# Kernel tuning notes

Measured on AMD Instinct MI355X. Metric: run time of the kernel, lower is better.

The kernel has to match this reference:

```python
import jax, jax.numpy as jnp
import numpy as np

EPS = 1e-8
LAMB = 0.5
L2_NORM = 1e-4
NUM_USERS = 100000
NUM_ITEMS = 50000
EMBED = 64
R = 3
NNZ = 1_000_000
IG_NNZ = 500_000
B = 512
K = 100


def _spmm(rows, cols, vals, X, num_rows):
    # sparse [num_rows, n] @ X  via gather + segment-sum
    return jax.ops.segment_sum(X[cols] * vals[:, None], rows, num_segments=num_rows)


def setup_inputs() -> dict:
    key = jax.random.key(0)
    ks = jax.random.split(key, 16)
    user = jax.random.randint(ks[0], (B,), 0, NUM_USERS)
    item = jax.random.randint(ks[1], (B, K), 0, NUM_ITEMS)
    rel_rows = jax.random.randint(ks[2], (R, NNZ), 0, NUM_USERS)
    rel_cols = jax.random.randint(ks[3], (R, NNZ), 0, NUM_ITEMS)
    ig_rows = jax.random.randint(ks[4], (R, IG_NNZ), 0, NUM_ITEMS)
    ig_cols = jax.random.randint(ks[5], (R, IG_NNZ), 0, NUM_ITEMS)
    ig_vals = jnp.ones((R, IG_NNZ), jnp.float32)
    train_rows = jax.random.randint(ks[6], (NNZ,), 0, NUM_USERS)
    train_cols = jax.random.randint(ks[7], (NNZ,), 0, NUM_ITEMS)
    user_embedding = 0.1 * jax.random.normal(ks[8], (NUM_USERS, EMBED), jnp.float32)
    item_embedding = 0.1 * jax.random.normal(ks[9], (NUM_ITEMS, EMBED), jnp.float32)
    mgnn_weight = jnp.ones((R,), jnp.float32)
    item_behavior_W = 0.05 * jax.random.normal(ks[10], (R, 2 * EMBED, 2 * EMBED), jnp.float32)
    item_propagate_W = 0.05 * jax.random.normal(ks[11], (R, EMBED, EMBED), jnp.float32)
    W = 0.05 * jax.random.normal(ks[12], (EMBED, EMBED), jnp.float32)
    return {"user": user, "item": item, "rel_rows": rel_rows, "rel_cols": rel_cols,
            "ig_rows": ig_rows, "ig_cols": ig_cols, "ig_vals": ig_vals,
            "train_rows": train_rows, "train_cols": train_cols,
            "user_embedding": user_embedding, "item_embedding": item_embedding,
            "mgnn_weight": mgnn_weight, "item_behavior_W": item_behavior_W,
            "item_propagate_W": item_propagate_W, "W": W}


def reference(user, item, rel_rows, rel_cols, ig_rows, ig_cols, ig_vals,
              train_rows, train_cols, user_embedding, item_embedding,
              mgnn_weight, item_behavior_W, item_propagate_W, W):
    # user behavior degree [U, R] (number of interactions per user per relation)
    ub_deg = jax.vmap(lambda r: jax.ops.segment_sum(
        jnp.ones(r.shape, jnp.float32), r, num_segments=NUM_USERS))(rel_rows).T
    total_weight = ub_deg @ mgnn_weight[:, None]                       # [U,1]
    user_behavior_weight = ub_deg * mgnn_weight[None, :] / (total_weight + EPS)

    user_feature = jnp.zeros((NUM_USERS, EMBED), user_embedding.dtype)
    score2 = jnp.zeros((item.shape[0], item.shape[1]), user_embedding.dtype)
    for i in range(R):
        # item-item propagation for relation i
        ig_deg = jax.ops.segment_sum(ig_vals[i], ig_rows[i], num_segments=NUM_ITEMS)[:, None]
        item_agg = _spmm(ig_rows[i], ig_cols[i], ig_vals[i], item_embedding, NUM_ITEMS)
        item_agg = item_agg / (ig_deg + EPS)
        tmp_item_prop = jnp.concatenate([item_embedding, item_agg @ item_propagate_W[i]], axis=1)  # [I,2E]

        ones = jnp.ones(rel_rows[i].shape, user_embedding.dtype)
        ub_d = ub_deg[:, i:i + 1]
        tmp_user_neigh = _spmm(rel_rows[i], rel_cols[i], ones, item_embedding, NUM_USERS) / (ub_d + EPS)
        tmp_user_item_p = _spmm(rel_rows[i], rel_cols[i], ones, tmp_item_prop, NUM_USERS) / (ub_d + EPS)

        user_feature = user_feature + user_behavior_weight[:, i:i + 1] * tmp_user_neigh
        proj = tmp_user_item_p @ item_behavior_W[i]                    # [U,2E]
        # score2 term: <proj[user], tmp_item_prop[item]> per candidate
        score2 = score2 + jnp.einsum('be,bke->bk', proj[user], tmp_item_prop[item])
    score2 = score2 / R

    # item feature from transposed train matrix (values=1, no node dropout)
    item_feature = jax.ops.segment_sum(user_embedding[train_rows], train_cols, num_segments=NUM_ITEMS)

    uf = jnp.concatenate([user_embedding, user_feature @ W], axis=1)   # [U,2E]
    itf = jnp.concatenate([item_embedding, item_feature @ W], axis=1)  # [I,2E]

    u_g = uf[user]                                                     # [B,2E]
    i_g = itf[item]                                                    # [B,K,2E]
    score1 = jnp.einsum('be,bke->bk', u_g, i_g)
    scores = score1 + LAMB * score2
    # L2 on expanded user feature [B,K,2E] and gathered item feature
    l2_loss = L2_NORM * (item.shape[1] * (u_g ** 2).sum() + (i_g ** 2).sum())
    return scores, l2_loss
```

## Files before the change

### kernel.cpp

```cpp
#include <hip/hip_runtime.h>

#define EPSF     1e-8f
#define LAMBF    0.5f
#define L2NORMF  1e-4f
#define NUSERS   100000
#define NITEMS   50000
#define EMB      64
#define RREL     3
#define NNZ_     1000000
#define IGNNZ    500000
#define BB       512
#define KK       100

#define IGTOT    (RREL * IGNNZ)
#define TOTE     (IGTOT + NNZ_)
#define NBIN_SEG 782
#define NBINS    (4 * NBIN_SEG)
#define NBLK     128
#define BTH      1024
#define SLICE    ((TOTE + NBLK - 1) / NBLK)
#define CAPE     2048
#define GTH      512

__global__ void scatter_maps(const int* __restrict__ user, const int* __restrict__ item,
                             int* __restrict__ slot, int* __restrict__ iflag) {
    int i = blockIdx.x * blockDim.x + threadIdx.x;
    if (i < BB) slot[user[i]] = i;
    if (i < BB * KK) iflag[item[i]] = 1;
}

__device__ __forceinline__ int edge_bin(int i, const int* ig_rows, const int* train_cols) {
    if (i < IGTOT) return (i / IGNNZ) * NBIN_SEG + (ig_rows[i] >> 6);
    return 3 * NBIN_SEG + (train_cols[i - IGTOT] >> 6);
}

__global__ void pass1_count(const int* __restrict__ ig_rows, const int* __restrict__ train_cols,
                            int* __restrict__ pcnt) {
    __shared__ int h[NBINS];
    int b = blockIdx.x, t = threadIdx.x;
    for (int i = t; i < NBINS; i += BTH) h[i] = 0;
    __syncthreads();
    int s = b * SLICE, e = min(s + SLICE, TOTE);
    for (int i = s + t; i < e; i += BTH)
        atomicAdd(&h[edge_bin(i, ig_rows, train_cols)], 1);
    __syncthreads();
    for (int i = t; i < NBINS; i += BTH) pcnt[b * NBINS + i] = h[i];
}

__global__ void scan_tot(const int* __restrict__ pcnt, int* __restrict__ tot) {
    int bin = blockIdx.x * blockDim.x + threadIdx.x;
    if (bin >= NBINS) return;
    int s = 0;
    for (int b = 0; b < NBLK; b++) s += pcnt[b * NBINS + bin];
    tot[bin] = s;
}

__global__ void scan_bins(const int* __restrict__ tot, int* __restrict__ binbase) {
    __shared__ int csum[1024];
    int t = threadIdx.x;
    int base = t * 4;
    int v0 = (base + 0 < NBINS) ? tot[base + 0] : 0;
    int v1 = (base + 1 < NBINS) ? tot[base + 1] : 0;
    int v2 = (base + 2 < NBINS) ? tot[base + 2] : 0;
    int v3 = (base + 3 < NBINS) ? tot[base + 3] : 0;
    int s = v0 + v1 + v2 + v3;
    csum[t] = s;
    __syncthreads();
    for (int d = 1; d < 1024; d <<= 1) {
        int x = (t >= d) ? csum[t - d] : 0;
        __syncthreads();
        csum[t] += x;
        __syncthreads();
    }
    int run = csum[t] - s;
    if (base + 0 < NBINS) { binbase[base + 0] = run; run += v0; }
    if (base + 1 < NBINS) { binbase[base + 1] = run; run += v1; }
    if (base + 2 < NBINS) { binbase[base + 2] = run; run += v2; }
    if (base + 3 < NBINS) { binbase[base + 3] = run; run += v3; }
    if (t == 0) binbase[NBINS] = TOTE;
}

__global__ void scan_obase(const int* __restrict__ pcnt, const int* __restrict__ binbase,
                           int* __restrict__ obase) {
    int bin = blockIdx.x * blockDim.x + threadIdx.x;
    if (bin >= NBINS) return;
    int run = binbase[bin];
    for (int b = 0; b < NBLK; b++) {
        obase[b * NBINS + bin] = run;
        run += pcnt[b * NBINS + bin];
    }
}

__global__ void pass2_scatter(const int* __restrict__ ig_rows, const int* __restrict__ ig_cols,
                              const float* __restrict__ ig_vals, const int* __restrict__ train_rows,
                              const int* __restrict__ train_cols, const int* __restrict__ obase,
                              int2* __restrict__ garr, int* __restrict__ tcol) {
    __shared__ int pos[NBINS];
    int b = blockIdx.x, t = threadIdx.x;
    for (int i = t; i < NBINS; i += BTH) pos[i] = obase[b * NBINS + i];
    __syncthreads();
    int s = b * SLICE, e = min(s + SLICE, TOTE);
    for (int i = s + t; i < e; i += BTH) {
        if (i < IGTOT) {
            int dest = ig_rows[i];
            int bin = (i / IGNNZ) * NBIN_SEG + (dest >> 6);
            int slot = atomicAdd(&pos[bin], 1);
            garr[slot] = make_int2((ig_cols[i] << 6) | (dest & 63),
                                   __float_as_int(ig_vals[i]));
        } else {
            int e2 = i - IGTOT;
            int dest = train_cols[e2];
            int bin = 3 * NBIN_SEG + (dest >> 6);
            int slot = atomicAdd(&pos[bin], 1);
            tcol[slot - IGTOT] = (train_rows[e2] << 6) | (dest & 63);
        }
    }
}

__device__ __forceinline__ void bin_scan(int t, int* cnt, int* off, int* pos) {
    if (t < 64) {
        int v = cnt[t];
        int inc = v;
#pragma unroll
        for (int d = 1; d < 64; d <<= 1) {
            int x = __shfl_up(inc, d);
            if (t >= d) inc += x;
        }
        off[t] = inc - v;
        pos[t] = inc - v;
        if (t == 63) off[64] = inc;
    }
}

__global__ void ig_bin_gather(const float* __restrict__ item_emb, const int* __restrict__ binbase,
                              const int2* __restrict__ garr, float* __restrict__ prop2, int seg) {
    __shared__ int scol[CAPE];
    __shared__ float sval[CAPE];
    __shared__ int cnt[64], off[65], pos[64];
    int t = threadIdx.x, w = t >> 6, lane = t & 63;
    int bin = seg * NBIN_SEG + blockIdx.x;
    int bstart = binbase[bin], bend = binbase[bin + 1];
    int n = bend - bstart;
    int row0 = blockIdx.x * 64;
    if (n <= CAPE) {
        if (t < 64) cnt[t] = 0;
        __syncthreads();
        for (int i = t; i < n; i += GTH) atomicAdd(&cnt[garr[bstart + i].x & 63], 1);
        __syncthreads();
        bin_scan(t, cnt, off, pos);
        __syncthreads();
        for (int i = t; i < n; i += GTH) {
            int2 pv = garr[bstart + i];
            int sl = atomicAdd(&pos[pv.x & 63], 1);
            scol[sl] = pv.x >> 6;
            sval[sl] = __int_as_float(pv.y);
        }
        __syncthreads();
        for (int r = w; r < 64; r += 8) {
            int grow = row0 + r;
            if (grow >= NITEMS) break;
            int s = off[r], e = off[r + 1];
            float acc = 0.f, deg = 0.f;
            for (int k = s; k < e; k += 8) {
                int i0 = min(k + 0, e - 1), i1 = min(k + 1, e - 1);
                int i2 = min(k + 2, e - 1), i3 = min(k + 3, e - 1);
                int i4 = min(k + 4, e - 1), i5 = min(k + 5, e - 1);
                int i6 = min(k + 6, e - 1), i7 = min(k + 7, e - 1);
                int c0 = scol[i0], c1 = scol[i1], c2 = scol[i2], c3 = scol[i3];
                int c4 = scol[i4], c5 = scol[i5], c6 = scol[i6], c7 = scol[i7];
                float v0 = (k + 0 < e) ? sval[i0] : 0.f, v1 = (k + 1 < e) ? sval[i1] : 0.f;
                float v2 = (k + 2 < e) ? sval[i2] : 0.f, v3 = (k + 3 < e) ? sval[i3] : 0.f;
                float v4 = (k + 4 < e) ? sval[i4] : 0.f, v5 = (k + 5 < e) ? sval[i5] : 0.f;
                float v6 = (k + 6 < e) ? sval[i6] : 0.f, v7 = (k + 7 < e) ? sval[i7] : 0.f;
                float f0 = item_emb[c0 * 64 + lane], f1 = item_emb[c1 * 64 + lane];
                float f2 = item_emb[c2 * 64 + lane], f3 = item_emb[c3 * 64 + lane];
                float f4 = item_emb[c4 * 64 + lane], f5 = item_emb[c5 * 64 + lane];
                float f6 = item_emb[c6 * 64 + lane], f7 = item_emb[c7 * 64 + lane];
                acc += v0 * f0 + v1 * f1 + v2 * f2 + v3 * f3
                     + v4 * f4 + v5 * f5 + v6 * f6 + v7 * f7;
                deg += (v0 + v1 + v2 + v3) + (v4 + v5 + v6 + v7);
            }
            prop2[grow * 64 + lane] = acc / (deg + EPSF);
        }
    } else {
        for (int r = w; r < 64; r += 8) {
            int grow = row0 + r;
            if (grow >= NITEMS) break;
            float acc = 0.f, deg = 0.f;
            for (int j0 = bstart; j0 < bend; j0 += 64) {
                int j = j0 + lane;
                int2 pv = (j < bend) ? garr[j] : make_int2(-1, 0);
                unsigned long long mask = __ballot(pv.x >= 0 && (pv.x & 63) == r);
                while (mask) {
                    int jj = __builtin_ctzll(mask); mask &= mask - 1;
                    int pj = __shfl(pv.x, jj);
                    float vj = __shfl(__int_as_float(pv.y), jj);
                    acc += vj * item_emb[(pj >> 6) * 64 + lane];
                    deg += vj;
                }
            }
            prop2[grow * 64 + lane] = acc / (deg + EPSF);
        }
    }
}

__global__ void train_bin_gather(const float* __restrict__ user_emb, const int* __restrict__ binbase,
                                 const int* __restrict__ tcol, const int* __restrict__ iflag,
                                 float* __restrict__ itf2) {
    __shared__ int scol[CAPE];
    __shared__ int cnt[64], off[65], pos[64];
    int t = threadIdx.x, w = t >> 6, lane = t & 63;
    int bin = 3 * NBIN_SEG + blockIdx.x;
    int bstart = binbase[bin] - IGTOT, bend = binbase[bin + 1] - IGTOT;
    int n = bend - bstart;
    int row0 = blockIdx.x * 64;
    if (n <= CAPE) {
        if (t < 64) cnt[t] = 0;
        __syncthreads();
        for (int i = t; i < n; i += GTH) atomicAdd(&cnt[tcol[bstart + i] & 63], 1);
        __syncthreads();
        bin_scan(t, cnt, off, pos);
        __syncthreads();
        for (int i = t; i < n; i += GTH) {
            int p = tcol[bstart + i];
            int sl = atomicAdd(&pos[p & 63], 1);
            scol[sl] = p >> 6;
        }
        __syncthreads();
        for (int r = w; r < 64; r += 8) {
            int grow = row0 + r;
            if (grow >= NITEMS) break;
            if (!iflag[grow]) continue;
            int s = off[r], e = off[r + 1];
            float acc = 0.f;
            for (int k = s; k < e; k += 8) {
                int i0 = min(k + 0, e - 1), i1 = min(k + 1, e - 1);
                int i2 = min(k + 2, e - 1), i3 = min(k + 3, e - 1);
                int i4 = min(k + 4, e - 1), i5 = min(k + 5, e - 1);
                int i6 = min(k + 6, e - 1), i7 = min(k + 7, e - 1);
                int c0 = scol[i0], c1 = scol[i1], c2 = scol[i2], c3 = scol[i3];
                int c4 = scol[i4], c5 = scol[i5], c6 = scol[i6], c7 = scol[i7];
                float m1 = (k + 1 < e) ? 1.f : 0.f, m2 = (k + 2 < e) ? 1.f : 0.f;
                float m3 = (k + 3 < e) ? 1.f : 0.f, m4 = (k + 4 < e) ? 1.f : 0.f;
                float m5 = (k + 5 < e) ? 1.f : 0.f, m6 = (k + 6 < e) ? 1.f : 0.f;
                float m7 = (k + 7 < e) ? 1.f : 0.f;
                float f0 = user_emb[c0 * 64 + lane], f1 = user_emb[c1 * 64 + lane];
                float f2 = user_emb[c2 * 64 + lane], f3 = user_emb[c3 * 64 + lane];
                float f4 = user_emb[c4 * 64 + lane], f5 = user_emb[c5 * 64 + lane];
                float f6 = user_emb[c6 * 64 + lane], f7 = user_emb[c7 * 64 + lane];
                acc += f0 + m1 * f1 + m2 * f2 + m3 * f3
                     + m4 * f4 + m5 * f5 + m6 * f6 + m7 * f7;
            }
            itf2[grow * 64 + lane] = acc;
        }
    } else {
        for (int r = w; r < 64; r += 8) {
            int grow = row0 + r;
            if (grow >= NITEMS) break;
            if (!iflag[grow]) continue;
            float acc = 0.f;
            for (int j0 = bstart; j0 < bend; j0 += 64) {
                int j = j0 + lane;
                int p = (j < bend) ? tcol[j] : -1;
                unsigned long long mask = __ballot(p >= 0 && (p & 63) == r);
                while (mask) {
                    int jj = __builtin_ctzll(mask); mask &= mask - 1;
                    int pj = __shfl(p, jj);
                    acc += user_emb[(pj >> 6) * 64 + lane];
                }
            }
            itf2[grow * 64 + lane] = acc;
        }
    }
}

__global__ void apply_w(float* __restrict__ A, const float* __restrict__ Wm,
                        const int* __restrict__ flag, int M) {
    __shared__ float sW[64 * 64];
    __shared__ float sA[4][64];
    int tid = threadIdx.x;
    for (int i = tid; i < 64 * 64; i += 256) sW[i] = Wm[i];
    int lr = tid >> 6, c = tid & 63;
    int row = blockIdx.x * 4 + lr;
    bool act = (row < M) && (!flag || flag[row]);
    if (act) sA[lr][c] = A[row * 64 + c];
    __syncthreads();
    if (act) {
        float o = 0.f;
#pragma unroll
        for (int k = 0; k < 64; k++) o += sA[lr][k] * sW[k * 64 + c];
        A[row * 64 + c] = o;
    }
}

__device__ __forceinline__ void rel_hit(int s, int c, int lane,
                                        const float* __restrict__ item_emb,
                                        const float* __restrict__ prop2,
                                        float* __restrict__ accN, float* __restrict__ accP,
                                        float* __restrict__ ubc) {
    unsigned long long mask = __ballot(s >= 0);
    while (mask) {
        int j = __builtin_ctzll(mask);
        mask &= mask - 1;
        int bs = __shfl(s, j);
        int bc = __shfl(c, j);
        atomicAdd(&accN[bs * EMB + lane], item_emb[bc * EMB + lane]);
        atomicAdd(&accP[bs * EMB + lane], prop2[bc * EMB + lane]);
        if (lane == 0) atomicAdd(&ubc[bs], 1.0f);
    }
}

__global__ void rel_scan(const int* __restrict__ rows, const int* __restrict__ cols,
                         const int* __restrict__ slot, const float* __restrict__ item_emb,
                         const float* __restrict__ prop2,
                         float* __restrict__ accN, float* __restrict__ accP,
                         float* __restrict__ ubc) {
    int lane = threadIdx.x & 63;
    int gw = (blockIdx.x * blockDim.x + threadIdx.x) >> 6;
    int nw = (gridDim.x * blockDim.x) >> 6;
    for (int ch = gw; ch < NNZ_ / 256; ch += nw) {
        int base = ch * 256 + lane * 4;
        int4 r4 = *reinterpret_cast<const int4*>(rows + base);
        int4 c4 = *reinterpret_cast<const int4*>(cols + base);
        int s0 = slot[r4.x], s1 = slot[r4.y], s2 = slot[r4.z], s3 = slot[r4.w];
        rel_hit(s0, c4.x, lane, item_emb, prop2, accN, accP, ubc);
        rel_hit(s1, c4.y, lane, item_emb, prop2, accN, accP, ubc);
        rel_hit(s2, c4.z, lane, item_emb, prop2, accN, accP, ubc);
        rel_hit(s3, c4.w, lane, item_emb, prop2, accN, accP, ubc);
    }
}

__global__ void proj_score2(const int* __restrict__ user, const int* __restrict__ slot,
                            const float* __restrict__ ubc, const float* __restrict__ acc_neigh,
                            const float* __restrict__ acc_prop, const float* __restrict__ Wb,
                            const int* __restrict__ item, const float* __restrict__ item_emb,
                            const float* __restrict__ item_prop2, float* __restrict__ score2) {
    int b = blockIdx.x;
    int tid = threadIdx.x;
    __shared__ float tbuf[128];
    __shared__ float p[128];
    int rep = slot[user[b]];
    float inv = 1.0f / (ubc[rep] + EPSF);
    if (tid < 64)       tbuf[tid] = acc_neigh[rep * 64 + tid] * inv;
    else if (tid < 128) tbuf[tid] = acc_prop[rep * 64 + (tid - 64)] * inv;
    __syncthreads();
    if (tid < 128) {
        float o = 0.f;
#pragma unroll 8
        for (int k = 0; k < 128; k++) o += tbuf[k] * Wb[k * 128 + tid];
        p[tid] = o;
    }
    __syncthreads();
    int wave = tid >> 6, lane = tid & 63;
    for (int k = wave; k < KK; k += 4) {
        int it = item[b * KK + k];
        float s = p[lane] * item_emb[it * 64 + lane] + p[64 + lane] * item_prop2[it * 64 + lane];
        for (int off = 32; off > 0; off >>= 1) s += __shfl_xor(s, off);
        if (lane == 0) score2[b * KK + k] += s;
    }
}

__global__ void final_k(const int* __restrict__ user, const int* __restrict__ item,
                        const int* __restrict__ slot, const float* __restrict__ ubc,
                        const float* __restrict__ acc_neigh, const float* __restrict__ mw,
                        const float* __restrict__ W, const float* __restrict__ user_emb,
                        const float* __restrict__ item_emb, const float* __restrict__ itf2,
                        const float* __restrict__ score2, float* __restrict__ out,
                        float* __restrict__ l2out) {
    int b = blockIdx.x;
    int tid = threadIdx.x;
    int wave = tid >> 6, lane = tid & 63;
    __shared__ float uf[64], u1[64], u2[64];
    __shared__ float red[4];
    int u = user[b];
    if (tid < 64) {
        int rep = slot[u];
        float w0 = mw[0], w1 = mw[1], w2 = mw[2];
        float c0 = ubc[0 * BB + rep], c1 = ubc[1 * BB + rep], c2 = ubc[2 * BB + rep];
        float invT = 1.0f / (c0 * w0 + c1 * w1 + c2 * w2 + EPSF);
        float f = (c0 * w0 * invT) / (c0 + EPSF) * acc_neigh[(0 * BB + rep) * 64 + tid]
                + (c1 * w1 * invT) / (c1 + EPSF) * acc_neigh[(1 * BB + rep) * 64 + tid]
                + (c2 * w2 * invT) / (c2 + EPSF) * acc_neigh[(2 * BB + rep) * 64 + tid];
        uf[tid] = f;
        u1[tid] = user_emb[u * 64 + tid];
    }
    __syncthreads();
    if (tid < 64) {
        float o = 0.f;
#pragma unroll
        for (int k = 0; k < 64; k++) o += uf[k] * W[k * 64 + tid];
        u2[tid] = o;
    }
    __syncthreads();
    float l2part = 0.f;
    for (int k = wave; k < KK; k += 4) {
        int it = item[b * KK + k];
        float e1 = item_emb[it * 64 + lane], e2 = itf2[it * 64 + lane];
        float s = u1[lane] * e1 + u2[lane] * e2;
        float q = e1 * e1 + e2 * e2;
        for (int off = 32; off > 0; off >>= 1) {
            s += __shfl_xor(s, off);
            q += __shfl_xor(q, off);
        }
        if (lane == 0) {
            out[b * KK + k] = s + LAMBF * (score2[b * KK + k] * (1.0f / (float)RREL));
            l2part += q;
        }
    }
    float su = u1[lane] * u1[lane] + u2[lane] * u2[lane];
    for (int off = 32; off > 0; off >>= 1) su += __shfl_xor(su, off);
    if (wave == 0 && lane == 0) l2part += (float)KK * su;
    if (lane == 0) red[wave] = l2part;
    __syncthreads();
    if (tid == 0) atomicAdd(l2out, L2NORMF * (red[0] + red[1] + red[2] + red[3]));
}

extern "C" void kernel_launch(void* const* d_in, const int* in_sizes, int n_in,
                              void* d_out, int out_size, void* d_ws, size_t ws_size,
                              hipStream_t stream) {
    const int*   user       = (const int*)d_in[0];
    const int*   item       = (const int*)d_in[1];
    const int*   rel_rows   = (const int*)d_in[2];
    const int*   rel_cols   = (const int*)d_in[3];
    const int*   ig_rows    = (const int*)d_in[4];
    const int*   ig_cols    = (const int*)d_in[5];
    const float* ig_vals    = (const float*)d_in[6];
    const int*   train_rows = (const int*)d_in[7];
    const int*   train_cols = (const int*)d_in[8];
    const float* user_emb   = (const float*)d_in[9];
    const float* item_emb   = (const float*)d_in[10];
    const float* mw         = (const float*)d_in[11];
    const float* Wb         = (const float*)d_in[12];
    const float* Wp         = (const float*)d_in[13];
    const float* W          = (const float*)d_in[14];
    float* out = (float*)d_out;

    float* ws = (float*)d_ws;
    size_t o = 0;
    int2*  garr       = (int2*)(ws + o); o += (size_t)IGTOT * 2;
    int*   tcol       = (int*)(ws + o); o += NNZ_;
    int*   user_slot  = (int*)(ws + o); o += NUSERS;
    int*   iflag      = (int*)(ws + o); o += NITEMS;
    int*   pcnt       = (int*)(ws + o); o += (size_t)NBLK * NBINS;
    int*   tot        = (int*)(ws + o); o += NBINS;
    int*   binbase    = (int*)(ws + o); o += NBINS + 1;
    int*   obase      = (int*)(ws + o); o += (size_t)NBLK * NBINS;
    float* item_prop2 = ws + o; o += (size_t)NITEMS * 64;
    float* acc_neigh  = ws + o; o += (size_t)RREL * BB * 64;
    float* acc_prop   = ws + o; o += (size_t)RREL * BB * 64;
    float* ubc        = ws + o; o += (size_t)RREL * BB;
    float* score2     = ws + o; o += (size_t)BB * KK;
    if (ws_size < o * sizeof(float)) return;

    size_t zero_zone = (size_t)RREL * BB * 64 * 2 + RREL * BB + BB * KK;

    hipMemsetAsync(user_slot, 0xFF, (size_t)NUSERS * 4, stream);
    hipMemsetAsync(iflag, 0, (size_t)NITEMS * 4, stream);
    hipMemsetAsync(acc_neigh, 0, zero_zone * 4, stream);
    hipMemsetAsync(out + (out_size - 1), 0, 4, stream);
    scatter_maps<<<(BB * KK + 255) / 256, 256, 0, stream>>>(user, item, user_slot, iflag);

    pass1_count<<<NBLK, BTH, 0, stream>>>(ig_rows, train_cols, pcnt);
    scan_tot<<<(NBINS + 255) / 256, 256, 0, stream>>>(pcnt, tot);
    scan_bins<<<1, 1024, 0, stream>>>(tot, binbase);
    scan_obase<<<(NBINS + 255) / 256, 256, 0, stream>>>(pcnt, binbase, obase);
    pass2_scatter<<<NBLK, BTH, 0, stream>>>(ig_rows, ig_cols, ig_vals, train_rows, train_cols,
                                            obase, garr, tcol);

    for (int i = 0; i < RREL; i++) {
        ig_bin_gather<<<NBIN_SEG, GTH, 0, stream>>>(item_emb, binbase, garr, item_prop2, i);
        apply_w<<<(NITEMS + 3) / 4, 256, 0, stream>>>(item_prop2, Wp + (size_t)i * 64 * 64,
                                                      nullptr, NITEMS);
        rel_scan<<<1024, 256, 0, stream>>>(rel_rows + (size_t)i * NNZ_, rel_cols + (size_t)i * NNZ_,
                                           user_slot, item_emb, item_prop2,
                                           acc_neigh + (size_t)i * BB * 64,
                                           acc_prop + (size_t)i * BB * 64, ubc + (size_t)i * BB);
        proj_score2<<<BB, 256, 0, stream>>>(user, user_slot, ubc + (size_t)i * BB,
                                            acc_neigh + (size_t)i * BB * 64,
                                            acc_prop + (size_t)i * BB * 64,
                                            Wb + (size_t)i * 128 * 128,
                                            item, item_emb, item_prop2, score2);
    }

    float* itf2 = item_prop2;
    train_bin_gather<<<NBIN_SEG, GTH, 0, stream>>>(user_emb, binbase, tcol, iflag, itf2);
    apply_w<<<(NITEMS + 3) / 4, 256, 0, stream>>>(itf2, W, iflag, NITEMS);
    final_k<<<BB, 256, 0, stream>>>(user, item, user_slot, ubc, acc_neigh, mw, W,
                                    user_emb, item_emb, itf2, score2,
                                    out, out + (out_size - 1));
}
```

Before: 592.9 us.

## Batch all relations into single fused-grid launches when workspace allows

When the workspace is large enough to hold separate propagation buffers for all three relations plus the train features, the per-relation loop of gather, weight-apply, relation scan and projection kernels is replaced by one launch each that covers every relation in a larger grid. This removes serial launch boundaries and lets small per-relation kernels fill the GPU. score2 accumulation now uses atomics because relations run concurrently. The histogram pass block count is also halved. It costs extra workspace memory and atomic traffic, and keeps a per-relation fallback path.

```diff
diff --git a/kernel.cpp b/kernel.cpp
--- a/kernel.cpp
+++ b/kernel.cpp
@@ -16,11 +16,13 @@
 #define TOTE     (IGTOT + NNZ_)
 #define NBIN_SEG 782
 #define NBINS    (4 * NBIN_SEG)
-#define NBLK     128
+#define NBLK     64
 #define BTH      1024
 #define SLICE    ((TOTE + NBLK - 1) / NBLK)
 #define CAPE     2048
 #define GTH      512
+#define BPM      ((NITEMS + 3) / 4)
+#define CHUNKS   ((NNZ_ + 255) / 256)
 
 __global__ void scatter_maps(const int* __restrict__ user, const int* __restrict__ item,
                              int* __restrict__ slot, int* __restrict__ iflag) {
@@ -132,157 +134,162 @@
     }
 }
 
-__global__ void ig_bin_gather(const float* __restrict__ item_emb, const int* __restrict__ binbase,
-                              const int2* __restrict__ garr, float* __restrict__ prop2, int seg) {
+__global__ void gather_all(const float* __restrict__ item_emb, const float* __restrict__ user_emb,
+                           const int* __restrict__ binbase, const int2* __restrict__ garr,
+                           const int* __restrict__ tcol, const int* __restrict__ iflag,
+                           float* __restrict__ prop2, size_t pstride, float* __restrict__ itf2,
+                           int seg_base) {
     __shared__ int scol[CAPE];
     __shared__ float sval[CAPE];
     __shared__ int cnt[64], off[65], pos[64];
     int t = threadIdx.x, w = t >> 6, lane = t & 63;
-    int bin = seg * NBIN_SEG + blockIdx.x;
-    int bstart = binbase[bin], bend = binbase[bin + 1];
-    int n = bend - bstart;
-    int row0 = blockIdx.x * 64;
-    if (n <= CAPE) {
-        if (t < 64) cnt[t] = 0;
-        __syncthreads();
-        for (int i = t; i < n; i += GTH) atomicAdd(&cnt[garr[bstart + i].x & 63], 1);
-        __syncthreads();
-        bin_scan(t, cnt, off, pos);
-        __syncthreads();
-        for (int i = t; i < n; i += GTH) {
-            int2 pv = garr[bstart + i];
-            int sl = atomicAdd(&pos[pv.x & 63], 1);
-            scol[sl] = pv.x >> 6;
-            sval[sl] = __int_as_float(pv.y);
-        }
-        __syncthreads();
-        for (int r = w; r < 64; r += 8) {
-            int grow = row0 + r;
-            if (grow >= NITEMS) break;
-            int s = off[r], e = off[r + 1];
-            float acc = 0.f, deg = 0.f;
-            for (int k = s; k < e; k += 8) {
-                int i0 = min(k + 0, e - 1), i1 = min(k + 1, e - 1);
-                int i2 = min(k + 2, e - 1), i3 = min(k + 3, e - 1);
-                int i4 = min(k + 4, e - 1), i5 = min(k + 5, e - 1);
-                int i6 = min(k + 6, e - 1), i7 = min(k + 7, e - 1);
-                int c0 = scol[i0], c1 = scol[i1], c2 = scol[i2], c3 = scol[i3];
-                int c4 = scol[i4], c5 = scol[i5], c6 = scol[i6], c7 = scol[i7];
-                float v0 = (k + 0 < e) ? sval[i0] : 0.f, v1 = (k + 1 < e) ? sval[i1] : 0.f;
-                float v2 = (k + 2 < e) ? sval[i2] : 0.f, v3 = (k + 3 < e) ? sval[i3] : 0.f;
-                float v4 = (k + 4 < e) ? sval[i4] : 0.f, v5 = (k + 5 < e) ? sval[i5] : 0.f;
-                float v6 = (k + 6 < e) ? sval[i6] : 0.f, v7 = (k + 7 < e) ? sval[i7] : 0.f;
-                float f0 = item_emb[c0 * 64 + lane], f1 = item_emb[c1 * 64 + lane];
-                float f2 = item_emb[c2 * 64 + lane], f3 = item_emb[c3 * 64 + lane];
-                float f4 = item_emb[c4 * 64 + lane], f5 = item_emb[c5 * 64 + lane];
-                float f6 = item_emb[c6 * 64 + lane], f7 = item_emb[c7 * 64 + lane];
-                acc += v0 * f0 + v1 * f1 + v2 * f2 + v3 * f3
-                     + v4 * f4 + v5 * f5 + v6 * f6 + v7 * f7;
-                deg += (v0 + v1 + v2 + v3) + (v4 + v5 + v6 + v7);
+    int seg = seg_base + blockIdx.x / NBIN_SEG;
+    int lbin = blockIdx.x % NBIN_SEG;
+    int bin = seg * NBIN_SEG + lbin;
+    int row0 = lbin * 64;
+    if (seg < 3) {
+        float* outp = prop2 + (size_t)(seg - seg_base) * pstride;
+        int bstart = binbase[bin], bend = binbase[bin + 1];
+        int n = bend - bstart;
+        if (n <= CAPE) {
+            if (t < 64) cnt[t] = 0;
+            __syncthreads();
+            for (int i = t; i < n; i += GTH) atomicAdd(&cnt[garr[bstart + i].x & 63], 1);
+            __syncthreads();
+            bin_scan(t, cnt, off, pos);
+            __syncthreads();
+            for (int i = t; i < n; i += GTH) {
+                int2 pv = garr[bstart + i];
+                int sl = atomicAdd(&pos[pv.x & 63], 1);
+                scol[sl] = pv.x >> 6;
+                sval[sl] = __int_as_float(pv.y);
             }
-            prop2[grow * 64 + lane] = acc / (deg + EPSF);
+            __syncthreads();
+            for (int r = w; r < 64; r += 8) {
+                int grow = row0 + r;
+                if (grow >= NITEMS) break;
+                int s = off[r], e = off[r + 1];
+                float acc = 0.f, deg = 0.f;
+                for (int k = s; k < e; k += 8) {
+                    int i0 = min(k + 0, e - 1), i1 = min(k + 1, e - 1);
+                    int i2 = min(k + 2, e - 1), i3 = min(k + 3, e - 1);
+                    int i4 = min(k + 4, e - 1), i5 = min(k + 5, e - 1);
+                    int i6 = min(k + 6, e - 1), i7 = min(k + 7, e - 1);
+                    int c0 = scol[i0], c1 = scol[i1], c2 = scol[i2], c3 = scol[i3];
+                    int c4 = scol[i4], c5 = scol[i5], c6 = scol[i6], c7 = scol[i7];
+                    float v0 = (k + 0 < e) ? sval[i0] : 0.f, v1 = (k + 1 < e) ? sval[i1] : 0.f;
+                    float v2 = (k + 2 < e) ? sval[i2] : 0.f, v3 = (k + 3 < e) ? sval[i3] : 0.f;
+                    float v4 = (k + 4 < e) ? sval[i4] : 0.f, v5 = (k + 5 < e) ? sval[i5] : 0.f;
+                    float v6 = (k + 6 < e) ? sval[i6] : 0.f, v7 = (k + 7 < e) ? sval[i7] : 0.f;
+                    float f0 = item_emb[c0 * 64 + lane], f1 = item_emb[c1 * 64 + lane];
+                    float f2 = item_emb[c2 * 64 + lane], f3 = item_emb[c3 * 64 + lane];
+                    float f4 = item_emb[c4 * 64 + lane], f5 = item_emb[c5 * 64 + lane];
+                    float f6 = item_emb[c6 * 64 + lane], f7 = item_emb[c7 * 64 + lane];
+                    acc += v0 * f0 + v1 * f1 + v2 * f2 + v3 * f3
+                         + v4 * f4 + v5 * f5 + v6 * f6 + v7 * f7;
+                    deg += (v0 + v1 + v2 + v3) + (v4 + v5 + v6 + v7);
+                }
+                outp[grow * 64 + lane] = acc / (deg + EPSF);
+            }
+        } else {
+            for (int r = w; r < 64; r += 8) {
+                int grow = row0 + r;
+                if (grow >= NITEMS) break;
+                float acc = 0.f, deg = 0.f;
+                for (int j0 = bstart; j0 < bend; j0 += 64) {
+                    int j = j0 + lane;
+                    int2 pv = (j < bend) ? garr[j] : make_int2(-1, 0);
+                    unsigned long long mask = __ballot(pv.x >= 0 && (pv.x & 63) == r);
+                    while (mask) {
+                        int jj = __builtin_ctzll(mask); mask &= mask - 1;
+                        int pj = __shfl(pv.x, jj);
+                        float vj = __shfl(__int_as_float(pv.y), jj);
+                        acc += vj * item_emb[(pj >> 6) * 64 + lane];
+                        deg += vj;
+                    }
+                }
+                outp[grow * 64 + lane] = acc / (deg + EPSF);
+            }
         }
     } else {
-        for (int r = w; r < 64; r += 8) {
-            int grow = row0 + r;
-            if (grow >= NITEMS) break;
-            float acc = 0.f, deg = 0.f;
-            for (int j0 = bstart; j0 < bend; j0 += 64) {
-                int j = j0 + lane;
-                int2 pv = (j < bend) ? garr[j] : make_int2(-1, 0);
-                unsigned long long mask = __ballot(pv.x >= 0 && (pv.x & 63) == r);
-                while (mask) {
-                    int jj = __builtin_ctzll(mask); mask &= mask - 1;
-                    int pj = __shfl(pv.x, jj);
-                    float vj = __shfl(__int_as_float(pv.y), jj);
-                    acc += vj * item_emb[(pj >> 6) * 64 + lane];
-                    deg += vj;
+        int bstart = binbase[bin] - IGTOT, bend = binbase[bin + 1] - IGTOT;
+        int n = bend - bstart;
+        if (n <= CAPE) {
+            if (t < 64) cnt[t] = 0;
+            __syncthreads();
+            for (int i = t; i < n; i += GTH) atomicAdd(&cnt[tcol[bstart + i] & 63], 1);
+            __syncthreads();
+            bin_scan(t, cnt, off, pos);
+            __syncthreads();
+            for (int i = t; i < n; i += GTH) {
+                int p = tcol[bstart + i];
+                int sl = atomicAdd(&pos[p & 63], 1);
+                scol[sl] = p >> 6;
+            }
+            __syncthreads();
+            for (int r = w; r < 64; r += 8) {
+                int grow = row0 + r;
+                if (grow >= NITEMS) break;
+                if (!iflag[grow]) continue;
+                int s = off[r], e = off[r + 1];
+                float acc = 0.f;
+                for (int k = s; k < e; k += 8) {
+                    int i0 = min(k + 0, e - 1), i1 = min(k + 1, e - 1);
+                    int i2 = min(k + 2, e - 1), i3 = min(k + 3, e - 1);
+                    int i4 = min(k + 4, e - 1), i5 = min(k + 5, e - 1);
+                    int i6 = min(k + 6, e - 1), i7 = min(k + 7, e - 1);
+                    int c0 = scol[i0], c1 = scol[i1], c2 = scol[i2], c3 = scol[i3];
+                    int c4 = scol[i4], c5 = scol[i5], c6 = scol[i6], c7 = scol[i7];
+                    float m1 = (k + 1 < e) ? 1.f : 0.f, m2 = (k + 2 < e) ? 1.f : 0.f;
+                    float m3 = (k + 3 < e) ? 1.f : 0.f, m4 = (k + 4 < e) ? 1.f : 0.f;
+                    float m5 = (k + 5 < e) ? 1.f : 0.f, m6 = (k + 6 < e) ? 1.f : 0.f;
+                    float m7 = (k + 7 < e) ? 1.f : 0.f;
+                    float f0 = user_emb[c0 * 64 + lane], f1 = user_emb[c1 * 64 + lane];
+                    float f2 = user_emb[c2 * 64 + lane], f3 = user_emb[c3 * 64 + lane];
+                    float f4 = user_emb[c4 * 64 + lane], f5 = user_emb[c5 * 64 + lane];
+                    float f6 = user_emb[c6 * 64 + lane], f7 = user_emb[c7 * 64 + lane];
+                    acc += f0 + m1 * f1 + m2 * f2 + m3 * f3
+                         + m4 * f4 + m5 * f5 + m6 * f6 + m7 * f7;
                 }
+                itf2[grow * 64 + lane] = acc;
             }
-            prop2[grow * 64 + lane] = acc / (deg + EPSF);
-        }
-    }
-}
-
-__global__ void train_bin_gather(const float* __restrict__ user_emb, const int* __restrict__ binbase,
-                                 const int* __restrict__ tcol, const int* __restrict__ iflag,
-                                 float* __restrict__ itf2) {
-    __shared__ int scol[CAPE];
-    __shared__ int cnt[64], off[65], pos[64];
-    int t = threadIdx.x, w = t >> 6, lane = t & 63;
-    int bin = 3 * NBIN_SEG + blockIdx.x;
-    int bstart = binbase[bin] - IGTOT, bend = binbase[bin + 1] - IGTOT;
-    int n = bend - bstart;
-    int row0 = blockIdx.x * 64;
-    if (n <= CAPE) {
-        if (t < 64) cnt[t] = 0;
-        __syncthreads();
-        for (int i = t; i < n; i += GTH) atomicAdd(&cnt[tcol[bstart + i] & 63], 1);
-        __syncthreads();
-        bin_scan(t, cnt, off, pos);
-        __syncthreads();
-        for (int i = t; i < n; i += GTH) {
-            int p = tcol[bstart + i];
-            int sl = atomicAdd(&pos[p & 63], 1);
-            scol[sl] = p >> 6;
-        }
-        __syncthreads();
-        for (int r = w; r < 64; r += 8) {
-            int grow = row0 + r;
-            if (grow >= NITEMS) break;
-            if (!iflag[grow]) continue;
-            int s = off[r], e = off[r + 1];
-            float acc = 0.f;
-            for (int k = s; k < e; k += 8) {
-                int i0 = min(k + 0, e - 1), i1 = min(k + 1, e - 1);
-                int i2 = min(k + 2, e - 1), i3 = min(k + 3, e - 1);
-                int i4 = min(k + 4, e - 1), i5 = min(k + 5, e - 1);
-                int i6 = min(k + 6, e - 1), i7 = min(k + 7, e - 1);
-                int c0 = scol[i0], c1 = scol[i1], c2 = scol[i2], c3 = scol[i3];
-                int c4 = scol[i4], c5 = scol[i5], c6 = scol[i6], c7 = scol[i7];
-                float m1 = (k + 1 < e) ? 1.f : 0.f, m2 = (k + 2 < e) ? 1.f : 0.f;
-                float m3 = (k + 3 < e) ? 1.f : 0.f, m4 = (k + 4 < e) ? 1.f : 0.f;
-                float m5 = (k + 5 < e) ? 1.f : 0.f, m6 = (k + 6 < e) ? 1.f : 0.f;
-                float m7 = (k + 7 < e) ? 1.f : 0.f;
-                float f0 = user_emb[c0 * 64 + lane], f1 = user_emb[c1 * 64 + lane];
-                float f2 = user_emb[c2 * 64 + lane], f3 = user_emb[c3 * 64 + lane];
-                float f4 = user_emb[c4 * 64 + lane], f5 = user_emb[c5 * 64 + lane];
-                float f6 = user_emb[c6 * 64 + lane], f7 = user_emb[c7 * 64 + lane];
-                acc += f0 + m1 * f1 + m2 * f2 + m3 * f3
-                     + m4 * f4 + m5 * f5 + m6 * f6 + m7 * f7;
+        } else {
+            for (int r = w; r < 64; r += 8) {
+                int grow = row0 + r;
+                if (grow >= NITEMS) break;
+                if (!iflag[grow]) continue;
+                float acc = 0.f;
+                for (int j0 = bstart; j0 < bend; j0 += 64) {
+                    int j = j0 + lane;
+                    int p = (j < bend) ? tcol[j] : -1;
+                    unsigned long long mask = __ballot(p >= 0 && (p & 63) == r);
+                    while (mask) {
+                        int jj = __builtin_ctzll(mask); mask &= mask - 1;
+                        int pj = __shfl(p, jj);
+                        acc += user_emb[(pj >> 6) * 64 + lane];
+                    }
+                }
+                itf2[grow * 64 + lane] = acc;
             }
-            itf2[grow * 64 + lane] = acc;
-        }
-    } else {
-        for (int r = w; r < 64; r += 8) {
-            int grow = row0 + r;
-            if (grow >= NITEMS) break;
-            if (!iflag[grow]) continue;
-            float acc = 0.f;
-            for (int j0 = bstart; j0 < bend; j0 += 64) {
-                int j = j0 + lane;
-                int p = (j < bend) ? tcol[j] : -1;
-                unsigned long long mask = __ballot(p >= 0 && (p & 63) == r);
-                while (mask) {
-                    int jj = __builtin_ctzll(mask); mask &= mask - 1;
-                    int pj = __shfl(p, jj);
-                    acc += user_emb[(pj >> 6) * 64 + lane];
-                }
-            }
-            itf2[grow * 64 + lane] = acc;
-        }
-    }
-}
-
-__global__ void apply_w(float* __restrict__ A, const float* __restrict__ Wm,
-                        const int* __restrict__ flag, int M) {
+        }
+    }
+}
+
+__global__ void apply_all(float* __restrict__ prop2, size_t pstride, float* __restrict__ itf2,
+                          const float* __restrict__ Wp, const float* __restrict__ W,
+                          const int* __restrict__ iflag, int m_base) {
     __shared__ float sW[64 * 64];
     __shared__ float sA[4][64];
     int tid = threadIdx.x;
+    int m = m_base + blockIdx.x / BPM;
+    int blk = blockIdx.x % BPM;
+    float* A; const float* Wm; const int* flag;
+    if (m < 3) { A = prop2 + (size_t)(m - m_base) * pstride; Wm = Wp + (size_t)m * 4096; flag = nullptr; }
+    else       { A = itf2; Wm = W; flag = iflag; }
     for (int i = tid; i < 64 * 64; i += 256) sW[i] = Wm[i];
     int lr = tid >> 6, c = tid & 63;
-    int row = blockIdx.x * 4 + lr;
-    bool act = (row < M) && (!flag || flag[row]);
+    int row = blk * 4 + lr;
+    bool act = (row < NITEMS) && (!flag || flag[row]);
     if (act) sA[lr][c] = A[row * 64 + c];
     __syncthreads();
     if (act) {
@@ -310,53 +317,69 @@
     }
 }
 
-__global__ void rel_scan(const int* __restrict__ rows, const int* __restrict__ cols,
-                         const int* __restrict__ slot, const float* __restrict__ item_emb,
-                         const float* __restrict__ prop2,
-                         float* __restrict__ accN, float* __restrict__ accP,
-                         float* __restrict__ ubc) {
+__global__ void rel_scan_all(const int* __restrict__ rel_rows, const int* __restrict__ rel_cols,
+                             const int* __restrict__ slot, const float* __restrict__ item_emb,
+                             const float* __restrict__ prop2, size_t pstride,
+                             float* __restrict__ accN, float* __restrict__ accP,
+                             float* __restrict__ ubc, int rel_base, int nrel) {
     int lane = threadIdx.x & 63;
     int gw = (blockIdx.x * blockDim.x + threadIdx.x) >> 6;
     int nw = (gridDim.x * blockDim.x) >> 6;
-    for (int ch = gw; ch < NNZ_ / 256; ch += nw) {
-        int base = ch * 256 + lane * 4;
+    for (int ch = gw; ch < nrel * CHUNKS; ch += nw) {
+        int rel = rel_base + ch / CHUNKS;
+        int lch = ch % CHUNKS;
+        const int* rows = rel_rows + (size_t)rel * NNZ_;
+        const int* cols = rel_cols + (size_t)rel * NNZ_;
+        const float* pr = prop2 + (size_t)(rel - rel_base) * pstride;
+        float* aN = accN + (size_t)rel * BB * 64;
+        float* aP = accP + (size_t)rel * BB * 64;
+        float* ub = ubc + (size_t)rel * BB;
+        int base = lch * 256 + lane * 4;
+        if (base >= NNZ_) continue;
         int4 r4 = *reinterpret_cast<const int4*>(rows + base);
         int4 c4 = *reinterpret_cast<const int4*>(cols + base);
         int s0 = slot[r4.x], s1 = slot[r4.y], s2 = slot[r4.z], s3 = slot[r4.w];
-        rel_hit(s0, c4.x, lane, item_emb, prop2, accN, accP, ubc);
-        rel_hit(s1, c4.y, lane, item_emb, prop2, accN, accP, ubc);
-        rel_hit(s2, c4.z, lane, item_emb, prop2, accN, accP, ubc);
-        rel_hit(s3, c4.w, lane, item_emb, prop2, accN, accP, ubc);
-    }
-}
-
-__global__ void proj_score2(const int* __restrict__ user, const int* __restrict__ slot,
-                            const float* __restrict__ ubc, const float* __restrict__ acc_neigh,
-                            const float* __restrict__ acc_prop, const float* __restrict__ Wb,
-                            const int* __restrict__ item, const float* __restrict__ item_emb,
-                            const float* __restrict__ item_prop2, float* __restrict__ score2) {
-    int b = blockIdx.x;
+        rel_hit(s0, c4.x, lane, item_emb, pr, aN, aP, ub);
+        rel_hit(s1, c4.y, lane, item_emb, pr, aN, aP, ub);
+        rel_hit(s2, c4.z, lane, item_emb, pr, aN, aP, ub);
+        rel_hit(s3, c4.w, lane, item_emb, pr, aN, aP, ub);
+    }
+}
+
+__global__ void proj_all(const int* __restrict__ user, const int* __restrict__ slot,
+                         const float* __restrict__ ubc_all, const float* __restrict__ accN_all,
+                         const float* __restrict__ accP_all, const float* __restrict__ Wb,
+                         const int* __restrict__ item, const float* __restrict__ item_emb,
+                         const float* __restrict__ prop2, size_t pstride,
+                         float* __restrict__ score2, int rel_base) {
+    int rel = rel_base + blockIdx.x / BB;
+    int b = blockIdx.x % BB;
     int tid = threadIdx.x;
     __shared__ float tbuf[128];
     __shared__ float p[128];
+    const float* ubc = ubc_all + (size_t)rel * BB;
+    const float* accN = accN_all + (size_t)rel * BB * 64;
+    const float* accP = accP_all + (size_t)rel * BB * 64;
+    const float* Wbr = Wb + (size_t)rel * 128 * 128;
+    const float* pr = prop2 + (size_t)(rel - rel_base) * pstride;
     int rep = slot[user[b]];
     float inv = 1.0f / (ubc[rep] + EPSF);
-    if (tid < 64)       tbuf[tid] = acc_neigh[rep * 64 + tid] * inv;
-    else if (tid < 128) tbuf[tid] = acc_prop[rep * 64 + (tid - 64)] * inv;
+    if (tid < 64)       tbuf[tid] = accN[rep * 64 + tid] * inv;
+    else if (tid < 128) tbuf[tid] = accP[rep * 64 + (tid - 64)] * inv;
     __syncthreads();
     if (tid < 128) {
         float o = 0.f;
 #pragma unroll 8
-        for (int k = 0; k < 128; k++) o += tbuf[k] * Wb[k * 128 + tid];
+        for (int k = 0; k < 128; k++) o += tbuf[k] * Wbr[k * 128 + tid];
         p[tid] = o;
     }
     __syncthreads();
     int wave = tid >> 6, lane = tid & 63;
     for (int k = wave; k < KK; k += 4) {
         int it = item[b * KK + k];
-        float s = p[lane] * item_emb[it * 64 + lane] + p[64 + lane] * item_prop2[it * 64 + lane];
+        float s = p[lane] * item_emb[it * 64 + lane] + p[64 + lane] * pr[it * 64 + lane];
         for (int off = 32; off > 0; off >>= 1) s += __shfl_xor(s, off);
-        if (lane == 0) score2[b * KK + k] += s;
+        if (lane == 0) atomicAdd(&score2[b * KK + k], s);
     }
 }
 
@@ -435,6 +458,8 @@
     const float* W          = (const float*)d_in[14];
     float* out = (float*)d_out;
 
+    const size_t PM = (size_t)NITEMS * 64;
+
     float* ws = (float*)d_ws;
     size_t o = 0;
     int2*  garr       = (int2*)(ws + o); o += (size_t)IGTOT * 2;
@@ -445,18 +470,23 @@
     int*   tot        = (int*)(ws + o); o += NBINS;
     int*   binbase    = (int*)(ws + o); o += NBINS + 1;
     int*   obase      = (int*)(ws + o); o += (size_t)NBLK * NBINS;
-    float* item_prop2 = ws + o; o += (size_t)NITEMS * 64;
-    float* acc_neigh  = ws + o; o += (size_t)RREL * BB * 64;
-    float* acc_prop   = ws + o; o += (size_t)RREL * BB * 64;
-    float* ubc        = ws + o; o += (size_t)RREL * BB;
-    float* score2     = ws + o; o += (size_t)BB * KK;
-    if (ws_size < o * sizeof(float)) return;
-
-    size_t zero_zone = (size_t)RREL * BB * 64 * 2 + RREL * BB + BB * KK;
+    size_t o_pref = o;
+    size_t zz = (size_t)RREL * BB * 64 * 2 + RREL * BB + BB * KK;
+    size_t need_small = o_pref + PM + zz;
+    size_t need_big   = o_pref + 4 * PM + zz;
+    bool big = (ws_size >= need_big * 4);
+    if (!big && ws_size < need_small * 4) return;
+
+    float* prop2 = ws + o;          o += big ? 3 * PM : PM;
+    float* itf2  = big ? ws + o : prop2;  if (big) o += PM;
+    float* acc_neigh = ws + o;      o += (size_t)RREL * BB * 64;
+    float* acc_prop  = ws + o;      o += (size_t)RREL * BB * 64;
+    float* ubc       = ws + o;      o += (size_t)RREL * BB;
+    float* score2    = ws + o;      o += (size_t)BB * KK;
 
     hipMemsetAsync(user_slot, 0xFF, (size_t)NUSERS * 4, stream);
     hipMemsetAsync(iflag, 0, (size_t)NITEMS * 4, stream);
-    hipMemsetAsync(acc_neigh, 0, zero_zone * 4, stream);
+    hipMemsetAsync(acc_neigh, 0, zz * 4, stream);
     hipMemsetAsync(out + (out_size - 1), 0, 4, stream);
     scatter_maps<<<(BB * KK + 255) / 256, 256, 0, stream>>>(user, item, user_slot, iflag);
 
@@ -467,24 +497,29 @@
     pass2_scatter<<<NBLK, BTH, 0, stream>>>(ig_rows, ig_cols, ig_vals, train_rows, train_cols,
                                             obase, garr, tcol);
 
-    for (int i = 0; i < RREL; i++) {
-        ig_bin_gather<<<NBIN_SEG, GTH, 0, stream>>>(item_emb, binbase, garr, item_prop2, i);
-        apply_w<<<(NITEMS + 3) / 4, 256, 0, stream>>>(item_prop2, Wp + (size_t)i * 64 * 64,
-                                                      nullptr, NITEMS);
-        rel_scan<<<1024, 256, 0, stream>>>(rel_rows + (size_t)i * NNZ_, rel_cols + (size_t)i * NNZ_,
-                                           user_slot, item_emb, item_prop2,
-                                           acc_neigh + (size_t)i * BB * 64,
-                                           acc_prop + (size_t)i * BB * 64, ubc + (size_t)i * BB);
-        proj_score2<<<BB, 256, 0, stream>>>(user, user_slot, ubc + (size_t)i * BB,
-                                            acc_neigh + (size_t)i * BB * 64,
-                                            acc_prop + (size_t)i * BB * 64,
-                                            Wb + (size_t)i * 128 * 128,
-                                            item, item_emb, item_prop2, score2);
-    }
-
-    float* itf2 = item_prop2;
-    train_bin_gather<<<NBIN_SEG, GTH, 0, stream>>>(user_emb, binbase, tcol, iflag, itf2);
-    apply_w<<<(NITEMS + 3) / 4, 256, 0, stream>>>(itf2, W, iflag, NITEMS);
+    if (big) {
+        gather_all<<<4 * NBIN_SEG, GTH, 0, stream>>>(item_emb, user_emb, binbase, garr, tcol,
+                                                     iflag, prop2, PM, itf2, 0);
+        apply_all<<<4 * BPM, 256, 0, stream>>>(prop2, PM, itf2, Wp, W, iflag, 0);
+        rel_scan_all<<<2048, 256, 0, stream>>>(rel_rows, rel_cols, user_slot, item_emb,
+                                               prop2, PM, acc_neigh, acc_prop, ubc, 0, RREL);
+        proj_all<<<RREL * BB, 256, 0, stream>>>(user, user_slot, ubc, acc_neigh, acc_prop, Wb,
+                                                item, item_emb, prop2, PM, score2, 0);
+    } else {
+        for (int i = 0; i < RREL; i++) {
+            gather_all<<<NBIN_SEG, GTH, 0, stream>>>(item_emb, user_emb, binbase, garr, tcol,
+                                                     iflag, prop2, 0, itf2, i);
+            apply_all<<<BPM, 256, 0, stream>>>(prop2, 0, itf2, Wp, W, iflag, i);
+            rel_scan_all<<<1024, 256, 0, stream>>>(rel_rows, rel_cols, user_slot, item_emb,
+                                                   prop2, 0, acc_neigh, acc_prop, ubc, i, 1);
+            proj_all<<<BB, 256, 0, stream>>>(user, user_slot, ubc, acc_neigh, acc_prop, Wb,
+                                             item, item_emb, prop2, 0, score2, i);
+        }
+        gather_all<<<NBIN_SEG, GTH, 0, stream>>>(item_emb, user_emb, binbase, garr, tcol,
+                                                 iflag, prop2, 0, itf2, 3);
+        apply_all<<<BPM, 256, 0, stream>>>(prop2, 0, itf2, Wp, W, iflag, 3);
+    }
+
     final_k<<<BB, 256, 0, stream>>>(user, item, user_slot, ubc, acc_neigh, mw, W,
                                     user_emb, item_emb, itf2, score2,
                                     out, out + (out_size - 1));
```

Result: faster. 516.1 us (-12.9%).
